# Kernel tuning notes

Measured on AMD Instinct MI355X. Metric: run time of the kernel, lower is better.

Reference implementation:

```python
import jax, jax.numpy as jnp
import numpy as np

K = 11        # filter_size
HALF = K // 2 # 5
N_ITER = 5
EPS = 1e-8


def setup_inputs() -> dict:
    key = jax.random.key(0)
    k1, k2 = jax.random.split(key)
    logits = jax.random.normal(k1, (16, 100000), dtype=jnp.float32)
    p = jax.random.normal(k2, (16, 100000, 3), dtype=jnp.float32)
    return {"logits": logits, "p": p}


def _shift_stack(x, offsets, n):
    # x: [B, C, N+2*HALF] padded; returns [B, len(offsets), C, N]
    return jnp.stack([x[:, :, d:d + n] for d in offsets], axis=1)


def reference(logits, p):
    B, N = logits.shape
    feat = jnp.transpose(p, (0, 2, 1))      # [B,3,N]  (p.permute(0,2,1))
    unary = logits[:, None, :]              # [B,1,N]  (logits.unsqueeze(1))

    offsets = [d for d in range(K) if d != HALF]  # exclude self-connection

    fpad = jnp.pad(feat, ((0, 0), (0, 0), (HALF, HALF)))
    mpad = jnp.pad(jnp.ones((B, 1, N), logits.dtype), ((0, 0), (0, 0), (HALF, HALF)))
    f_sh = _shift_stack(fpad, offsets, N)   # [B,10,3,N]
    m_sh = _shift_stack(mpad, offsets, N)   # [B,10,1,N] valid mask (zero outside seq)

    # Gaussian pairwise kernel on point features, fixed across iterations
    w = jnp.exp(-0.5 * jnp.sum((feat[:, None] - f_sh) ** 2, axis=2, keepdims=True)) * m_sh  # [B,10,1,N]
    wsum = jnp.sum(w, axis=1) + EPS         # [B,1,N]

    def body(q, _):
        qpad = jnp.pad(q, ((0, 0), (0, 0), (HALF, HALF)))
        q_sh = _shift_stack(qpad, offsets, N)          # [B,10,1,N]
        msg = jnp.sum(w * q_sh, axis=1) / wsum          # normalized message
        q_new = jax.nn.sigmoid(unary + msg)             # mean-field update
        return q_new, None

    q0 = jax.nn.sigmoid(unary)
    q, _ = jax.lax.scan(body, q0, None, length=N_ITER)
    return q[:, 0, :]  # .squeeze() -> [B,N] marginal probabilities
```

## Files before the change

kernel.cpp:

```cpp
#include <hip/hip_runtime.h>


constexpr int BLK   = 64;
constexpr int G     = 4;
constexpr int E     = BLK * G;
constexpr int HL    = 28;
constexpr int C     = E - 2 * HL;
constexpr int NITER = 5;
constexpr float EPS = 1e-8f;

__device__ __forceinline__ float frcp(float x) { return __builtin_amdgcn_rcpf(x); }
__device__ __forceinline__ float sigm(float x) { return frcp(1.0f + __expf(-x)); }

__global__ __launch_bounds__(BLK, 4) void crf_kernel(
    const float* __restrict__ logits, const float* __restrict__ p,
    float* __restrict__ out, int N, int chunks_per_b)
{
  __shared__ float4 s_q4[BLK];

  const int b     = blockIdx.x / chunks_per_b;
  const int chunk = blockIdx.x % chunks_per_b;
  const int s0    = chunk * C - HL;
  const int t     = threadIdx.x;
  const int gb    = s0 + G * t;
  const float* lg = logits + (size_t)b * N;
  const float* pp = p + (size_t)b * N * 3;

  const bool interior = (s0 >= 5) && (s0 + E + 5 < N);

  float fx[14][3];
  if (interior) {
    float own[12];
    const float4* vp = (const float4*)(pp + 3 * gb);
    float4 v0 = vp[0], v1 = vp[1], v2 = vp[2];
    own[0] = v0.x; own[1]  = v0.y; own[2]  = v0.z; own[3]  = v0.w;
    own[4] = v1.x; own[5]  = v1.y; own[6]  = v1.z; own[7]  = v1.w;
    own[8] = v2.x; own[9]  = v2.y; own[10] = v2.z; own[11] = v2.w;
    #pragma unroll
    for (int c = 0; c < 3; ++c) fx[0][c] = __shfl_up(own[9 + c], 2);
    #pragma unroll
    for (int j = 0; j < 4; ++j)
      #pragma unroll
      for (int c = 0; c < 3; ++c) fx[1 + j][c] = __shfl_up(own[3 * j + c], 1);
    #pragma unroll
    for (int j = 0; j < 4; ++j)
      #pragma unroll
      for (int c = 0; c < 3; ++c) fx[5 + j][c] = own[3 * j + c];
    #pragma unroll
    for (int j = 0; j < 4; ++j)
      #pragma unroll
      for (int c = 0; c < 3; ++c) fx[9 + j][c] = __shfl_down(own[3 * j + c], 1);
    #pragma unroll
    for (int c = 0; c < 3; ++c) fx[13][c] = __shfl_down(own[c], 2);
  } else {
    #pragma unroll
    for (int j = 0; j < 14; ++j) {
      int g  = gb + j - 5;
      int gc = min(max(g, 0), N - 1);
      const float* src = pp + 3 * (size_t)gc;
      fx[j][0] = src[0]; fx[j][1] = src[1]; fx[j][2] = src[2];
    }
  }

  float wr[G][5], wl[G][5];
  #pragma unroll
  for (int i = 0; i < 9; ++i) {
    #pragma unroll
    for (int d = 0; d < 5; ++d) {
      float d0 = fx[i][0] - fx[i + d + 1][0];
      float d1 = fx[i][1] - fx[i + d + 1][1];
      float d2 = fx[i][2] - fx[i + d + 1][2];
      float ex = __expf(-0.5f * (d0 * d0 + d1 * d1 + d2 * d2));
      if (!interior) {
        int g = gb + i - 5;
        ex = (g >= 0 && g + d + 1 < N) ? ex : 0.0f;
      }
      if (i >= 5) wr[i - 5][d] = ex;
      const int kl = i + d - 4;
      if (kl >= 0 && kl < G) wl[kl][d] = ex;
    }
  }

  float un[G], q[G];
  if (interior) {
    float4 u = *(const float4*)(lg + gb);
    un[0] = u.x; un[1] = u.y; un[2] = u.z; un[3] = u.w;
  } else {
    #pragma unroll
    for (int k = 0; k < G; ++k) un[k] = lg[min(max(gb + k, 0), N - 1)];
  }
  #pragma unroll
  for (int k = 0; k < G; ++k) {
    float ws = EPS;
    #pragma unroll
    for (int d = 0; d < 5; ++d) ws += wr[k][d] + wl[k][d];
    float inv = frcp(ws);
    #pragma unroll
    for (int d = 0; d < 5; ++d) { wr[k][d] *= inv; wl[k][d] *= inv; }
    q[k] = sigm(un[k]);
  }

  const int tL1 = max(t - 1, 0), tL2 = max(t - 2, 0);
  const int tR1 = min(t + 1, BLK - 1), tR2 = min(t + 2, BLK - 1);

  s_q4[t] = make_float4(q[0], q[1], q[2], q[3]);
  __syncthreads();

  #pragma unroll
  for (int it = 0; it < NITER; ++it) {
    float4 L2 = s_q4[tL2];
    float4 L1 = s_q4[tL1];
    float4 R1 = s_q4[tR1];
    float4 R2 = s_q4[tR2];
    float qx[14];
    qx[0] = L2.w;
    qx[1] = L1.x; qx[2]  = L1.y; qx[3]  = L1.z; qx[4]  = L1.w;
    qx[5] = q[0]; qx[6]  = q[1]; qx[7]  = q[2]; qx[8]  = q[3];
    qx[9] = R1.x; qx[10] = R1.y; qx[11] = R1.z; qx[12] = R1.w;
    qx[13] = R2.x;

    #pragma unroll
    for (int k = 0; k < G; ++k) {
      float msg = 0.0f;
      #pragma unroll
      for (int d = 0; d < 5; ++d) {
        msg += wl[k][d] * qx[5 + k - d - 1];
        msg += wr[k][d] * qx[5 + k + d + 1];
      }
      q[k] = sigm(un[k] + msg);
    }

    if (it != NITER - 1) {
      __syncthreads();
      s_q4[t] = make_float4(q[0], q[1], q[2], q[3]);
      __syncthreads();
    }
  }

  const int e0 = G * t;
  if (e0 >= HL && e0 + G <= E - HL) {
    const int gx = chunk * C + (e0 - HL);
    float* ob = out + (size_t)b * N + gx;
    float4 v = make_float4(q[0], q[1], q[2], q[3]);
    if (gx + 3 < N) {
      *(float4*)ob = v;
    } else {
      #pragma unroll
      for (int j = 0; j < 4; ++j)
        if (gx + j < N) ob[j] = (&v.x)[j];
    }
  }
}

extern "C" void kernel_launch(void* const* d_in, const int* in_sizes, int n_in,
                              void* d_out, int out_size, void* d_ws, size_t ws_size,
                              hipStream_t stream) {
  const float* logits = (const float*)d_in[0];
  const float* p      = (const float*)d_in[1];
  float* out          = (float*)d_out;
  const int N = 100000;
  const int B = in_sizes[0] / N;
  const int chunks_per_b = (N + C - 1) / C;
  dim3 grid(B * chunks_per_b), block(BLK);
  crf_kernel<<<grid, block, 0, stream>>>(logits, p, out, N, chunks_per_b);
}
```

Measured before the change: 19.01 us.

## Replace shared-memory halo exchange with wavefront shuffles and share pairwise weights

```diff
diff --git a/kernel.cpp b/kernel.cpp
--- a/kernel.cpp
+++ b/kernel.cpp
@@ -16,10 +16,8 @@
     const float* __restrict__ logits, const float* __restrict__ p,
     float* __restrict__ out, int N, int chunks_per_b)
 {
-  __shared__ float4 s_q4[BLK];
-
   const int b     = blockIdx.x / chunks_per_b;
-  const int chunk = blockIdx.x % chunks_per_b;
+  const int chunk = blockIdx.x - b * chunks_per_b;
   const int s0    = chunk * C - HL;
   const int t     = threadIdx.x;
   const int gb    = s0 + G * t;
@@ -28,96 +26,92 @@
 
   const bool interior = (s0 >= 5) && (s0 + E + 5 < N);
 
-  float fx[14][3];
+  float own[12], un[G];
   if (interior) {
-    float own[12];
     const float4* vp = (const float4*)(pp + 3 * gb);
     float4 v0 = vp[0], v1 = vp[1], v2 = vp[2];
     own[0] = v0.x; own[1]  = v0.y; own[2]  = v0.z; own[3]  = v0.w;
     own[4] = v1.x; own[5]  = v1.y; own[6]  = v1.z; own[7]  = v1.w;
     own[8] = v2.x; own[9]  = v2.y; own[10] = v2.z; own[11] = v2.w;
-    #pragma unroll
-    for (int c = 0; c < 3; ++c) fx[0][c] = __shfl_up(own[9 + c], 2);
-    #pragma unroll
-    for (int j = 0; j < 4; ++j)
-      #pragma unroll
-      for (int c = 0; c < 3; ++c) fx[1 + j][c] = __shfl_up(own[3 * j + c], 1);
-    #pragma unroll
-    for (int j = 0; j < 4; ++j)
-      #pragma unroll
-      for (int c = 0; c < 3; ++c) fx[5 + j][c] = own[3 * j + c];
-    #pragma unroll
-    for (int j = 0; j < 4; ++j)
-      #pragma unroll
-      for (int c = 0; c < 3; ++c) fx[9 + j][c] = __shfl_down(own[3 * j + c], 1);
-    #pragma unroll
-    for (int c = 0; c < 3; ++c) fx[13][c] = __shfl_down(own[c], 2);
-  } else {
-    #pragma unroll
-    for (int j = 0; j < 14; ++j) {
-      int g  = gb + j - 5;
-      int gc = min(max(g, 0), N - 1);
-      const float* src = pp + 3 * (size_t)gc;
-      fx[j][0] = src[0]; fx[j][1] = src[1]; fx[j][2] = src[2];
-    }
-  }
-
-  float wr[G][5], wl[G][5];
-  #pragma unroll
-  for (int i = 0; i < 9; ++i) {
-    #pragma unroll
-    for (int d = 0; d < 5; ++d) {
-      float d0 = fx[i][0] - fx[i + d + 1][0];
-      float d1 = fx[i][1] - fx[i + d + 1][1];
-      float d2 = fx[i][2] - fx[i + d + 1][2];
-      float ex = __expf(-0.5f * (d0 * d0 + d1 * d1 + d2 * d2));
-      if (!interior) {
-        int g = gb + i - 5;
-        ex = (g >= 0 && g + d + 1 < N) ? ex : 0.0f;
-      }
-      if (i >= 5) wr[i - 5][d] = ex;
-      const int kl = i + d - 4;
-      if (kl >= 0 && kl < G) wl[kl][d] = ex;
-    }
-  }
-
-  float un[G], q[G];
-  if (interior) {
     float4 u = *(const float4*)(lg + gb);
     un[0] = u.x; un[1] = u.y; un[2] = u.z; un[3] = u.w;
   } else {
     #pragma unroll
-    for (int k = 0; k < G; ++k) un[k] = lg[min(max(gb + k, 0), N - 1)];
+    for (int k = 0; k < G; ++k) {
+      int gc = min(max(gb + k, 0), N - 1);
+      own[3 * k + 0] = pp[3 * (size_t)gc + 0];
+      own[3 * k + 1] = pp[3 * (size_t)gc + 1];
+      own[3 * k + 2] = pp[3 * (size_t)gc + 2];
+      un[k] = lg[gc];
+    }
   }
+
+  float fh[5][3];
+  #pragma unroll
+  for (int j = 0; j < 4; ++j)
+    #pragma unroll
+    for (int c = 0; c < 3; ++c)
+      fh[j][c] = __shfl_down(own[3 * j + c], 1);
+  #pragma unroll
+  for (int c = 0; c < 3; ++c)
+    fh[4][c] = __shfl_down(own[c], 2);
+
+  float ww[G][5];
+  #pragma unroll
+  for (int k = 0; k < G; ++k) {
+    #pragma unroll
+    for (int d = 0; d < 5; ++d) {
+      const int j = k + d + 1;
+      float p0 = (j < 4) ? own[3 * j + 0] : fh[j - 4][0];
+      float p1 = (j < 4) ? own[3 * j + 1] : fh[j - 4][1];
+      float p2 = (j < 4) ? own[3 * j + 2] : fh[j - 4][2];
+      float d0 = own[3 * k + 0] - p0;
+      float d1 = own[3 * k + 1] - p1;
+      float d2 = own[3 * k + 2] - p2;
+      float ex = __expf(-0.5f * (d0 * d0 + d1 * d1 + d2 * d2));
+      if (!interior)
+        ex = (gb + k >= 0 && gb + k + d + 1 < N) ? ex : 0.0f;
+      ww[k][d] = ex;
+    }
+  }
+
+  float wl[G][5];
+  #pragma unroll
+  for (int k = 0; k < G; ++k) {
+    #pragma unroll
+    for (int d = 0; d < 5; ++d) {
+      const int s = k - d - 1;
+      float v;
+      if (s >= 0)       v = ww[s][d];
+      else if (s >= -4) v = __shfl_up(ww[s + 4][d], 1);
+      else              v = __shfl_up(ww[3][d], 2);
+      wl[k][d] = v;
+    }
+  }
+
+  float q[G];
   #pragma unroll
   for (int k = 0; k < G; ++k) {
     float ws = EPS;
     #pragma unroll
-    for (int d = 0; d < 5; ++d) ws += wr[k][d] + wl[k][d];
+    for (int d = 0; d < 5; ++d) ws += ww[k][d] + wl[k][d];
     float inv = frcp(ws);
     #pragma unroll
-    for (int d = 0; d < 5; ++d) { wr[k][d] *= inv; wl[k][d] *= inv; }
+    for (int d = 0; d < 5; ++d) { ww[k][d] *= inv; wl[k][d] *= inv; }
     q[k] = sigm(un[k]);
   }
 
-  const int tL1 = max(t - 1, 0), tL2 = max(t - 2, 0);
-  const int tR1 = min(t + 1, BLK - 1), tR2 = min(t + 2, BLK - 1);
-
-  s_q4[t] = make_float4(q[0], q[1], q[2], q[3]);
-  __syncthreads();
-
   #pragma unroll
   for (int it = 0; it < NITER; ++it) {
-    float4 L2 = s_q4[tL2];
-    float4 L1 = s_q4[tL1];
-    float4 R1 = s_q4[tR1];
-    float4 R2 = s_q4[tR2];
     float qx[14];
-    qx[0] = L2.w;
-    qx[1] = L1.x; qx[2]  = L1.y; qx[3]  = L1.z; qx[4]  = L1.w;
-    qx[5] = q[0]; qx[6]  = q[1]; qx[7]  = q[2]; qx[8]  = q[3];
-    qx[9] = R1.x; qx[10] = R1.y; qx[11] = R1.z; qx[12] = R1.w;
-    qx[13] = R2.x;
+    qx[0] = __shfl_up(q[3], 2);
+    #pragma unroll
+    for (int j = 0; j < 4; ++j) qx[1 + j] = __shfl_up(q[j], 1);
+    #pragma unroll
+    for (int k = 0; k < G; ++k) qx[5 + k] = q[k];
+    #pragma unroll
+    for (int j = 0; j < 4; ++j) qx[9 + j] = __shfl_down(q[j], 1);
+    qx[13] = __shfl_down(q[0], 2);
 
     #pragma unroll
     for (int k = 0; k < G; ++k) {
@@ -125,15 +119,9 @@
       #pragma unroll
       for (int d = 0; d < 5; ++d) {
         msg += wl[k][d] * qx[5 + k - d - 1];
-        msg += wr[k][d] * qx[5 + k + d + 1];
+        msg += ww[k][d] * qx[5 + k + d + 1];
       }
       q[k] = sigm(un[k] + msg);
-    }
-
-    if (it != NITER - 1) {
-      __syncthreads();
-      s_q4[t] = make_float4(q[0], q[1], q[2], q[3]);
-      __syncthreads();
     }
   }
 
```

New measurement: 16.92 us. 1.12x faster.
